# Performance work log

Measured on AMD Instinct MI355X. Metric: run time of the kernel, lower is better.

## Reference

```python
import jax, jax.numpy as jnp
import numpy as np

B, S, D_MODEL, H = 4, 1024, 768, 12
DEPTH = D_MODEL // H  # 64


def setup_inputs() -> dict:
    key = jax.random.key(0)
    ks = jax.random.split(key, 11)
    sd = 1.0 / np.sqrt(D_MODEL)
    return {
        "q": jax.random.normal(ks[0], (B, S, D_MODEL), jnp.float32),
        "k": jax.random.normal(ks[1], (B, S, D_MODEL), jnp.float32),
        "v": jax.random.normal(ks[2], (B, S, D_MODEL), jnp.float32),
        # NOTE: source uses [Dense(depth)] * num_heads -> ONE shared layer per q/k/v
        "Wq": jax.random.normal(ks[3], (D_MODEL, DEPTH), jnp.float32) * sd,
        "bq": jnp.zeros((DEPTH,), jnp.float32),
        "Wk": jax.random.normal(ks[4], (D_MODEL, DEPTH), jnp.float32) * sd,
        "bk": jnp.zeros((DEPTH,), jnp.float32),
        "Wv": jax.random.normal(ks[5], (D_MODEL, DEPTH), jnp.float32) * sd,
        "bv": jnp.zeros((DEPTH,), jnp.float32),
        "Wc": jax.random.normal(ks[6], (D_MODEL, D_MODEL), jnp.float32) * sd,
        "bc": jnp.zeros((D_MODEL,), jnp.float32),
    }


def reference(q, k, v, Wq, bq, Wk, bk, Wv, bv, Wc, bc):
    # All heads share the same weights (list * num_heads aliasing in source),
    # so compute one head and replicate. Heads produce identical outputs.
    qh = q @ Wq + bq  # [B, S, depth]
    kh = k @ Wk + bk
    vh = v @ Wv + bv
    # Source bug reproduced: dk = tf.shape(k)[1] on [B,H,S,depth] == num_heads
    scale = 1.0 / jnp.sqrt(jnp.float32(H))
    scores = jnp.einsum('bqd,bkd->bqk', qh, kh) * scale  # [B, S, S]
    weights = jax.nn.softmax(scores, axis=-1)
    oh = jnp.einsum('bqk,bkd->bqd', weights, vh)  # [B, S, depth]
    # concat of H identical heads along feature dim -> tile
    concat = jnp.tile(oh, (1, 1, H))  # [B, S, d_model]
    output = concat @ Wc + bc
    attention_weights = jnp.broadcast_to(weights[:, None], (B, H, S, S))
    return (output, attention_weights)
```

## Files before the change

kernel.cpp:

```cpp
#include <hip/hip_runtime.h>
#include <math.h>

#define BB 4
#define SS 1024
#define DM 768
#define HH 12
#define DEPTH 64
#define QBLK 8
#define PROWS 16
#define NROWS (BB * SS)

typedef float vfloat4 __attribute__((ext_vector_type(4)));
typedef short bf16x8 __attribute__((ext_vector_type(8)));
typedef float f32x4 __attribute__((ext_vector_type(4)));

__device__ inline ushort f2bf(float x) {
    uint u = __float_as_uint(x);
    u += 0x7FFFu + ((u >> 16) & 1u);
    return (ushort)(u >> 16);
}

__global__ __launch_bounds__(256, 3) void proj_kernel(
    const float* __restrict__ q, const float* __restrict__ k, const float* __restrict__ v,
    const float* __restrict__ Wq, const float* __restrict__ bq,
    const float* __restrict__ Wk, const float* __restrict__ bk,
    const float* __restrict__ Wv, const float* __restrict__ bv,
    float* __restrict__ qh, ushort* __restrict__ khu, ushort* __restrict__ vhu)
{
    __shared__ __align__(16) float rows[PROWS][DM];
    const int nrb  = NROWS / PROWS;
    const int m    = blockIdx.x / nrb;
    const int rb   = blockIdx.x % nrb;
    const int row0 = rb * PROWS;
    const int t    = threadIdx.x;

    const float* src  = (m == 0) ? q  : (m == 1) ? k  : v;
    const float* W    = (m == 0) ? Wq : (m == 1) ? Wk : Wv;
    const float* bias = (m == 0) ? bq : (m == 1) ? bk : bv;

    const float4* s4 = (const float4*)(src + (size_t)row0 * DM);
    float4* r4 = (float4*)&rows[0][0];
    for (int i = t; i < PROWS * DM / 4; i += 256) r4[i] = s4[i];
    __syncthreads();

    const int d  = t & 63;
    const int rg = t >> 6;
    const float* Wp = W + d;
    float a0 = bias[d], a1 = a0, a2 = a0, a3 = a0;
    #pragma unroll 8
    for (int i = 0; i < DM; i += 4) {
        const float wv0 = Wp[(size_t)(i + 0) * DEPTH];
        const float wv1 = Wp[(size_t)(i + 1) * DEPTH];
        const float wv2 = Wp[(size_t)(i + 2) * DEPTH];
        const float wv3 = Wp[(size_t)(i + 3) * DEPTH];
        const float4 r0 = *(const float4*)&rows[rg * 4 + 0][i];
        const float4 r1 = *(const float4*)&rows[rg * 4 + 1][i];
        const float4 r2 = *(const float4*)&rows[rg * 4 + 2][i];
        const float4 r3 = *(const float4*)&rows[rg * 4 + 3][i];
        a0 = fmaf(r0.x, wv0, a0); a0 = fmaf(r0.y, wv1, a0); a0 = fmaf(r0.z, wv2, a0); a0 = fmaf(r0.w, wv3, a0);
        a1 = fmaf(r1.x, wv0, a1); a1 = fmaf(r1.y, wv1, a1); a1 = fmaf(r1.z, wv2, a1); a1 = fmaf(r1.w, wv3, a1);
        a2 = fmaf(r2.x, wv0, a2); a2 = fmaf(r2.y, wv1, a2); a2 = fmaf(r2.z, wv2, a2); a2 = fmaf(r2.w, wv3, a2);
        a3 = fmaf(r3.x, wv0, a3); a3 = fmaf(r3.y, wv1, a3); a3 = fmaf(r3.z, wv2, a3); a3 = fmaf(r3.w, wv3, a3);
    }
    const size_t base = (size_t)(row0 + rg * 4) * DEPTH + d;
    if (m == 0) {
        float* dp = qh + base;
        dp[0] = a0; dp[DEPTH] = a1; dp[2 * DEPTH] = a2; dp[3 * DEPTH] = a3;
    } else {
        ushort* du = ((m == 1) ? khu : vhu) + base;
        du[0] = f2bf(a0); du[DEPTH] = f2bf(a1); du[2 * DEPTH] = f2bf(a2); du[3 * DEPTH] = f2bf(a3);
    }
}

__global__ __launch_bounds__(256) void wcred_kernel(
    const float* __restrict__ Wc, float* __restrict__ Wr)
{
    int idx = blockIdx.x * 256 + threadIdx.x;
    if (idx >= DEPTH * DM) return;
    int d = idx / DM, j = idx % DM;
    float s = 0.f;
    #pragma unroll
    for (int h = 0; h < HH; ++h)
        s += Wc[(size_t)(h * DEPTH + d) * DM + j];
    Wr[idx] = s;
}

__global__ __launch_bounds__(512, 4) void attn_core(
    const float* __restrict__ qh, const ushort* __restrict__ khu, const ushort* __restrict__ vhu,
    const float* __restrict__ Wr, const float* __restrict__ bc,
    float* __restrict__ out, float* __restrict__ attn)
{
    __shared__ __align__(16) ushort qf[16 * 72];
    __shared__ __align__(16) ushort kvbuf[256 * 72];
    __shared__ __align__(16) ushort pf[16 * 1032];
    __shared__ float redmax[16 * 8];
    __shared__ float redsum[16 * 8];

    const int t = threadIdx.x, l = t & 63, wid = t >> 6;
    const int li = l & 15, g4 = l >> 4;
    const int blk = blockIdx.x, b = blk >> 7;
    const int q0 = (blk & 127) * QBLK;
    const int key = t >> 1, hf = t & 1;

    {
        const int qq = t >> 6, dd = t & 63;
        qf[qq * 72 + dd] = f2bf(qh[((size_t)b * SS + q0 + qq) * DEPTH + dd] * 0.28867513459481287f);
        for (int i = t; i < 8 * 72; i += 512) qf[8 * 72 + i] = 0;
        for (int i = t; i < 8 * 1032; i += 512) pf[8 * 1032 + i] = 0;
    }

    const ushort* khb = khu + (size_t)b * SS * DEPTH;
    const ushort* vhb = vhu + (size_t)b * SS * DEPTH;

    uint4 kr0, kr1, kr2, kr3;
    {
        const uint4* g = (const uint4*)(khb + (size_t)key * DEPTH + hf * 32);
        kr0 = g[0]; kr1 = g[1]; kr2 = g[2]; kr3 = g[3];
    }
    __syncthreads();

    const bf16x8 a0 = *(const bf16x8*)&qf[li * 72 + g4 * 8];
    const bf16x8 a1 = *(const bf16x8*)&qf[li * 72 + 32 + g4 * 8];

    f32x4 c[8];
    #pragma unroll
    for (int i = 0; i < 8; ++i) c[i] = (f32x4){0.f, 0.f, 0.f, 0.f};

    #pragma unroll
    for (int s = 0; s < 4; ++s) {
        if (s) __syncthreads();
        {
            uint4* d4 = (uint4*)&kvbuf[key * 72 + hf * 32];
            d4[0] = kr0; d4[1] = kr1; d4[2] = kr2; d4[3] = kr3;
        }
        if (s < 3) {
            const uint4* g = (const uint4*)(khb + (size_t)((s + 1) * 256 + key) * DEPTH + hf * 32);
            kr0 = g[0]; kr1 = g[1]; kr2 = g[2]; kr3 = g[3];
        }
        __syncthreads();
        __builtin_amdgcn_s_setprio(1);
        #pragma unroll
        for (int jj = 0; jj < 2; ++jj) {
            const int tl = wid + 8 * jj;
            const int ci = 2 * s + jj;
            const bf16x8 b0 = *(const bf16x8*)&kvbuf[(tl * 16 + li) * 72 + g4 * 8];
            const bf16x8 b1 = *(const bf16x8*)&kvbuf[(tl * 16 + li) * 72 + 32 + g4 * 8];
            c[ci] = __builtin_amdgcn_mfma_f32_16x16x32_bf16(a0, b0, c[ci], 0, 0, 0);
            c[ci] = __builtin_amdgcn_mfma_f32_16x16x32_bf16(a1, b1, c[ci], 0, 0, 0);
        }
        __builtin_amdgcn_s_setprio(0);
    }

    bf16x8 vr0, vr1, vr2, vr3;
    {
        const bf16x8* g = (const bf16x8*)(vhb + (size_t)key * DEPTH + hf * 32);
        vr0 = g[0]; vr1 = g[1]; vr2 = g[2]; vr3 = g[3];
    }

    float mx[4], sm[4], inv[4];
    #pragma unroll
    for (int r = 0; r < 4; ++r) {
        float m_ = c[0][r];
        #pragma unroll
        for (int i = 1; i < 8; ++i) m_ = fmaxf(m_, c[i][r]);
        #pragma unroll
        for (int off = 1; off < 16; off <<= 1) m_ = fmaxf(m_, __shfl_xor(m_, off));
        mx[r] = m_;
    }
    if (li == 0) {
        #pragma unroll
        for (int r = 0; r < 4; ++r) redmax[(4 * g4 + r) * 8 + wid] = mx[r];
    }
    __syncthreads();
    #pragma unroll
    for (int r = 0; r < 4; ++r) {
        float m_ = redmax[(4 * g4 + r) * 8];
        #pragma unroll
        for (int w2 = 1; w2 < 8; ++w2) m_ = fmaxf(m_, redmax[(4 * g4 + r) * 8 + w2]);
        mx[r] = m_;
        sm[r] = 0.f;
    }
    #pragma unroll
    for (int i = 0; i < 8; ++i) {
        #pragma unroll
        for (int r = 0; r < 4; ++r) {
            const float e = __expf(c[i][r] - mx[r]);
            c[i][r] = e;
            sm[r] += e;
        }
    }
    #pragma unroll
    for (int r = 0; r < 4; ++r) {
        float s_ = sm[r];
        #pragma unroll
        for (int off = 1; off < 16; off <<= 1) s_ += __shfl_xor(s_, off);
        sm[r] = s_;
    }
    if (li == 0) {
        #pragma unroll
        for (int r = 0; r < 4; ++r) redsum[(4 * g4 + r) * 8 + wid] = sm[r];
    }
    __syncthreads();
    #pragma unroll
    for (int r = 0; r < 4; ++r) {
        float s_ = 0.f;
        #pragma unroll
        for (int w2 = 0; w2 < 8; ++w2) s_ += redsum[(4 * g4 + r) * 8 + w2];
        inv[r] = 1.f / s_;
    }
    if (l < 32) {
        #pragma unroll
        for (int i = 0; i < 8; ++i) {
            const int colbase = (16 * (i >> 1) + wid + 8 * (i & 1)) * 16 + li;
            #pragma unroll
            for (int r = 0; r < 4; ++r)
                pf[(4 * g4 + r) * 1032 + colbase] = f2bf(c[i][r] * inv[r]);
        }
    }
    __syncthreads();

    f32x4 cp = {0.f, 0.f, 0.f, 0.f};
    const int dt = wid >> 1, par = wid & 1;
    ushort* VT = kvbuf;
    #pragma unroll
    for (int s = 0; s < 4; ++s) {
        if (s) __syncthreads();
        {
            #pragma unroll
            for (int i = 0; i < 8; ++i) {
                VT[(hf * 32 + i     ) * 264 + key] = (ushort)vr0[i];
                VT[(hf * 32 + 8 + i ) * 264 + key] = (ushort)vr1[i];
                VT[(hf * 32 + 16 + i) * 264 + key] = (ushort)vr2[i];
                VT[(hf * 32 + 24 + i) * 264 + key] = (ushort)vr3[i];
            }
        }
        if (s < 3) {
            const bf16x8* g = (const bf16x8*)(vhb + (size_t)((s + 1) * 256 + key) * DEPTH + hf * 32);
            vr0 = g[0]; vr1 = g[1]; vr2 = g[2]; vr3 = g[3];
        }
        __syncthreads();
        __builtin_amdgcn_s_setprio(1);
        #pragma unroll
        for (int c2 = 0; c2 < 4; ++c2) {
            const int cc = par + 2 * c2;
            const bf16x8 ap = *(const bf16x8*)&pf[li * 1032 + s * 256 + cc * 32 + g4 * 8];
            const bf16x8 bv = *(const bf16x8*)&VT[(dt * 16 + li) * 264 + cc * 32 + g4 * 8];
            cp = __builtin_amdgcn_mfma_f32_16x16x32_bf16(ap, bv, cp, 0, 0, 0);
        }
        __builtin_amdgcn_s_setprio(0);
    }
    __syncthreads();

    float* part_f = (float*)kvbuf;
    float* ohT_f  = ((float*)kvbuf) + 2048;
    #pragma unroll
    for (int r = 0; r < 4; ++r) part_f[wid * 256 + r * 64 + l] = cp[r];
    __syncthreads();
    {
        const int qq = t >> 6, dd = t & 63;
        const int ls = (qq >> 2) * 16 + (dd & 15), rr = qq & 3, w0 = (dd >> 4) * 2;
        ohT_f[dd * 12 + qq] = part_f[w0 * 256 + rr * 64 + ls] + part_f[(w0 + 1) * 256 + rr * 64 + ls];
    }
    __syncthreads();

    for (int j = t; j < DM; j += 512) {
        float a[QBLK];
        const float bj = bc[j];
        #pragma unroll
        for (int r = 0; r < QBLK; ++r) a[r] = bj;
        const float* wc = Wr + j;
        #pragma unroll 16
        for (int d2 = 0; d2 < DEPTH; ++d2) {
            const float wv = wc[(size_t)d2 * DM];
            const float4 o0 = *(const float4*)&ohT_f[d2 * 12];
            const float4 o1 = *(const float4*)&ohT_f[d2 * 12 + 4];
            a[0] = fmaf(o0.x, wv, a[0]); a[1] = fmaf(o0.y, wv, a[1]);
            a[2] = fmaf(o0.z, wv, a[2]); a[3] = fmaf(o0.w, wv, a[3]);
            a[4] = fmaf(o1.x, wv, a[4]); a[5] = fmaf(o1.y, wv, a[5]);
            a[6] = fmaf(o1.z, wv, a[6]); a[7] = fmaf(o1.w, wv, a[7]);
        }
        float* ob = out + ((size_t)b * SS + q0) * DM + j;
        #pragma unroll
        for (int r = 0; r < QBLK; ++r)
            __builtin_nontemporal_store(a[r], ob + (size_t)r * DM);
    }

    {
        const int qq = t >> 6, c0 = t & 63;
        const ushort* prow = &pf[qq * 1032];
        float* abase = attn + ((size_t)(b * HH) * SS + (q0 + qq)) * SS;
        #pragma unroll
        for (int i = 0; i < 4; ++i) {
            const int col = i * 256 + c0 * 4;
            vfloat4 v4;
            v4.x = __uint_as_float((uint)prow[col + 0] << 16);
            v4.y = __uint_as_float((uint)prow[col + 1] << 16);
            v4.z = __uint_as_float((uint)prow[col + 2] << 16);
            v4.w = __uint_as_float((uint)prow[col + 3] << 16);
            #pragma unroll
            for (int h = 0; h < HH; ++h)
                __builtin_nontemporal_store(v4, (vfloat4*)(abase + (size_t)h * SS * SS + col));
        }
    }
}

extern "C" void kernel_launch(void* const* d_in, const int* in_sizes, int n_in,
                              void* d_out, int out_size, void* d_ws, size_t ws_size,
                              hipStream_t stream) {
    const float* q  = (const float*)d_in[0];
    const float* k  = (const float*)d_in[1];
    const float* v  = (const float*)d_in[2];
    const float* Wq = (const float*)d_in[3];
    const float* bq = (const float*)d_in[4];
    const float* Wk = (const float*)d_in[5];
    const float* bk = (const float*)d_in[6];
    const float* Wv = (const float*)d_in[7];
    const float* bv = (const float*)d_in[8];
    const float* Wc = (const float*)d_in[9];
    const float* bc = (const float*)d_in[10];

    float* out  = (float*)d_out;
    float* attn = out + (size_t)BB * SS * DM;

    float* ws = (float*)d_ws;
    const size_t NPROJ = (size_t)NROWS * DEPTH;
    float* qh   = ws;
    ushort* khu = (ushort*)(ws + NPROJ);
    ushort* vhu = (ushort*)(ws + NPROJ + NPROJ / 2);
    float* Wr   = ws + 2 * NPROJ;

    wcred_kernel<<<(DEPTH * DM + 255) / 256, 256, 0, stream>>>(Wc, Wr);
    proj_kernel<<<3 * (NROWS / PROWS), 256, 0, stream>>>(q, k, v, Wq, bq, Wk, bk, Wv, bv, qh, khu, vhu);
    attn_core<<<BB * (SS / QBLK), 512, 0, stream>>>(qh, khu, vhu, Wr, bc, out, attn);
}
```

Measured before the change: 100.1 us.

## Process 16 query rows per block with 1024 threads in attention core

Doubles the query block from 8 to 16 rows and the workgroup from 512 to 1024 threads, so the 16x16 MFMA tiles no longer carry zero-padded rows. K/V tiles are each loaded once per 16 queries instead of 8, halving staging traffic and the number of blocks. Work is redistributed so each of 16 waves handles one key tile per stage, with reductions widened to 16 waves. Larger blocks reduce the number of blocks and may lower occupancy flexibility.

```diff
diff --git a/kernel.cpp b/kernel.cpp
--- a/kernel.cpp
+++ b/kernel.cpp
@@ -6,7 +6,7 @@
 #define DM 768
 #define HH 12
 #define DEPTH 64
-#define QBLK 8
+#define QBLK 16
 #define PROWS 16
 #define NROWS (BB * SS)
 
@@ -85,7 +85,7 @@
     Wr[idx] = s;
 }
 
-__global__ __launch_bounds__(512, 4) void attn_core(
+__global__ __launch_bounds__(1024, 4) void attn_core(
     const float* __restrict__ qh, const ushort* __restrict__ khu, const ushort* __restrict__ vhu,
     const float* __restrict__ Wr, const float* __restrict__ bc,
     float* __restrict__ out, float* __restrict__ attn)
@@ -93,68 +93,63 @@
     __shared__ __align__(16) ushort qf[16 * 72];
     __shared__ __align__(16) ushort kvbuf[256 * 72];
     __shared__ __align__(16) ushort pf[16 * 1032];
-    __shared__ float redmax[16 * 8];
-    __shared__ float redsum[16 * 8];
+    __shared__ float redmax[16 * 16];
+    __shared__ float redsum[16 * 16];
 
     const int t = threadIdx.x, l = t & 63, wid = t >> 6;
     const int li = l & 15, g4 = l >> 4;
-    const int blk = blockIdx.x, b = blk >> 7;
-    const int q0 = (blk & 127) * QBLK;
-    const int key = t >> 1, hf = t & 1;
+    const int blk = blockIdx.x, b = blk >> 6;
+    const int q0 = (blk & 63) * QBLK;
+    const int key = t >> 2, qu = t & 3;
 
     {
         const int qq = t >> 6, dd = t & 63;
         qf[qq * 72 + dd] = f2bf(qh[((size_t)b * SS + q0 + qq) * DEPTH + dd] * 0.28867513459481287f);
-        for (int i = t; i < 8 * 72; i += 512) qf[8 * 72 + i] = 0;
-        for (int i = t; i < 8 * 1032; i += 512) pf[8 * 1032 + i] = 0;
     }
 
     const ushort* khb = khu + (size_t)b * SS * DEPTH;
     const ushort* vhb = vhu + (size_t)b * SS * DEPTH;
 
-    uint4 kr0, kr1, kr2, kr3;
-    {
-        const uint4* g = (const uint4*)(khb + (size_t)key * DEPTH + hf * 32);
-        kr0 = g[0]; kr1 = g[1]; kr2 = g[2]; kr3 = g[3];
+    uint4 kr0, kr1;
+    {
+        const uint4* g = (const uint4*)(khb + (size_t)key * DEPTH + qu * 16);
+        kr0 = g[0]; kr1 = g[1];
     }
     __syncthreads();
 
     const bf16x8 a0 = *(const bf16x8*)&qf[li * 72 + g4 * 8];
     const bf16x8 a1 = *(const bf16x8*)&qf[li * 72 + 32 + g4 * 8];
 
-    f32x4 c[8];
-    #pragma unroll
-    for (int i = 0; i < 8; ++i) c[i] = (f32x4){0.f, 0.f, 0.f, 0.f};
+    f32x4 c[4];
+    #pragma unroll
+    for (int i = 0; i < 4; ++i) c[i] = (f32x4){0.f, 0.f, 0.f, 0.f};
 
     #pragma unroll
     for (int s = 0; s < 4; ++s) {
         if (s) __syncthreads();
         {
-            uint4* d4 = (uint4*)&kvbuf[key * 72 + hf * 32];
-            d4[0] = kr0; d4[1] = kr1; d4[2] = kr2; d4[3] = kr3;
+            uint4* d4 = (uint4*)&kvbuf[key * 72 + qu * 16];
+            d4[0] = kr0; d4[1] = kr1;
         }
         if (s < 3) {
-            const uint4* g = (const uint4*)(khb + (size_t)((s + 1) * 256 + key) * DEPTH + hf * 32);
-            kr0 = g[0]; kr1 = g[1]; kr2 = g[2]; kr3 = g[3];
+            const uint4* g = (const uint4*)(khb + (size_t)((s + 1) * 256 + key) * DEPTH + qu * 16);
+            kr0 = g[0]; kr1 = g[1];
         }
         __syncthreads();
         __builtin_amdgcn_s_setprio(1);
-        #pragma unroll
-        for (int jj = 0; jj < 2; ++jj) {
-            const int tl = wid + 8 * jj;
-            const int ci = 2 * s + jj;
-            const bf16x8 b0 = *(const bf16x8*)&kvbuf[(tl * 16 + li) * 72 + g4 * 8];
-            const bf16x8 b1 = *(const bf16x8*)&kvbuf[(tl * 16 + li) * 72 + 32 + g4 * 8];
-            c[ci] = __builtin_amdgcn_mfma_f32_16x16x32_bf16(a0, b0, c[ci], 0, 0, 0);
-            c[ci] = __builtin_amdgcn_mfma_f32_16x16x32_bf16(a1, b1, c[ci], 0, 0, 0);
+        {
+            const bf16x8 b0 = *(const bf16x8*)&kvbuf[(wid * 16 + li) * 72 + g4 * 8];
+            const bf16x8 b1 = *(const bf16x8*)&kvbuf[(wid * 16 + li) * 72 + 32 + g4 * 8];
+            c[s] = __builtin_amdgcn_mfma_f32_16x16x32_bf16(a0, b0, c[s], 0, 0, 0);
+            c[s] = __builtin_amdgcn_mfma_f32_16x16x32_bf16(a1, b1, c[s], 0, 0, 0);
         }
         __builtin_amdgcn_s_setprio(0);
     }
 
-    bf16x8 vr0, vr1, vr2, vr3;
-    {
-        const bf16x8* g = (const bf16x8*)(vhb + (size_t)key * DEPTH + hf * 32);
-        vr0 = g[0]; vr1 = g[1]; vr2 = g[2]; vr3 = g[3];
+    bf16x8 vr0, vr1;
+    {
+        const bf16x8* g = (const bf16x8*)(vhb + (size_t)key * DEPTH + qu * 16);
+        vr0 = g[0]; vr1 = g[1];
     }
 
     float mx[4], sm[4], inv[4];
@@ -162,26 +157,26 @@
     for (int r = 0; r < 4; ++r) {
         float m_ = c[0][r];
         #pragma unroll
-        for (int i = 1; i < 8; ++i) m_ = fmaxf(m_, c[i][r]);
+        for (int i = 1; i < 4; ++i) m_ = fmaxf(m_, c[i][r]);
         #pragma unroll
         for (int off = 1; off < 16; off <<= 1) m_ = fmaxf(m_, __shfl_xor(m_, off));
         mx[r] = m_;
     }
     if (li == 0) {
         #pragma unroll
-        for (int r = 0; r < 4; ++r) redmax[(4 * g4 + r) * 8 + wid] = mx[r];
+        for (int r = 0; r < 4; ++r) redmax[(4 * g4 + r) * 16 + wid] = mx[r];
     }
     __syncthreads();
     #pragma unroll
     for (int r = 0; r < 4; ++r) {
-        float m_ = redmax[(4 * g4 + r) * 8];
-        #pragma unroll
-        for (int w2 = 1; w2 < 8; ++w2) m_ = fmaxf(m_, redmax[(4 * g4 + r) * 8 + w2]);
+        float m_ = redmax[(4 * g4 + r) * 16];
+        #pragma unroll
+        for (int w2 = 1; w2 < 16; ++w2) m_ = fmaxf(m_, redmax[(4 * g4 + r) * 16 + w2]);
         mx[r] = m_;
         sm[r] = 0.f;
     }
     #pragma unroll
-    for (int i = 0; i < 8; ++i) {
+    for (int i = 0; i < 4; ++i) {
         #pragma unroll
         for (int r = 0; r < 4; ++r) {
             const float e = __expf(c[i][r] - mx[r]);
@@ -198,29 +193,27 @@
     }
     if (li == 0) {
         #pragma unroll
-        for (int r = 0; r < 4; ++r) redsum[(4 * g4 + r) * 8 + wid] = sm[r];
+        for (int r = 0; r < 4; ++r) redsum[(4 * g4 + r) * 16 + wid] = sm[r];
     }
     __syncthreads();
     #pragma unroll
     for (int r = 0; r < 4; ++r) {
         float s_ = 0.f;
         #pragma unroll
-        for (int w2 = 0; w2 < 8; ++w2) s_ += redsum[(4 * g4 + r) * 8 + w2];
+        for (int w2 = 0; w2 < 16; ++w2) s_ += redsum[(4 * g4 + r) * 16 + w2];
         inv[r] = 1.f / s_;
     }
-    if (l < 32) {
-        #pragma unroll
-        for (int i = 0; i < 8; ++i) {
-            const int colbase = (16 * (i >> 1) + wid + 8 * (i & 1)) * 16 + li;
-            #pragma unroll
-            for (int r = 0; r < 4; ++r)
-                pf[(4 * g4 + r) * 1032 + colbase] = f2bf(c[i][r] * inv[r]);
-        }
+    #pragma unroll
+    for (int i = 0; i < 4; ++i) {
+        const int colbase = (i * 16 + wid) * 16 + li;
+        #pragma unroll
+        for (int r = 0; r < 4; ++r)
+            pf[(4 * g4 + r) * 1032 + colbase] = f2bf(c[i][r] * inv[r]);
     }
     __syncthreads();
 
     f32x4 cp = {0.f, 0.f, 0.f, 0.f};
-    const int dt = wid >> 1, par = wid & 1;
+    const int dt = wid >> 2, par = wid & 3;
     ushort* VT = kvbuf;
     #pragma unroll
     for (int s = 0; s < 4; ++s) {
@@ -228,23 +221,22 @@
         {
             #pragma unroll
             for (int i = 0; i < 8; ++i) {
-                VT[(hf * 32 + i     ) * 264 + key] = (ushort)vr0[i];
-                VT[(hf * 32 + 8 + i ) * 264 + key] = (ushort)vr1[i];
-                VT[(hf * 32 + 16 + i) * 264 + key] = (ushort)vr2[i];
-                VT[(hf * 32 + 24 + i) * 264 + key] = (ushort)vr3[i];
+                VT[(qu * 16 + i    ) * 266 + key] = (ushort)vr0[i];
+                VT[(qu * 16 + 8 + i) * 266 + key] = (ushort)vr1[i];
             }
         }
         if (s < 3) {
-            const bf16x8* g = (const bf16x8*)(vhb + (size_t)((s + 1) * 256 + key) * DEPTH + hf * 32);
-            vr0 = g[0]; vr1 = g[1]; vr2 = g[2]; vr3 = g[3];
+            const bf16x8* g = (const bf16x8*)(vhb + (size_t)((s + 1) * 256 + key) * DEPTH + qu * 16);
+            vr0 = g[0]; vr1 = g[1];
         }
         __syncthreads();
         __builtin_amdgcn_s_setprio(1);
         #pragma unroll
-        for (int c2 = 0; c2 < 4; ++c2) {
-            const int cc = par + 2 * c2;
-            const bf16x8 ap = *(const bf16x8*)&pf[li * 1032 + s * 256 + cc * 32 + g4 * 8];
-            const bf16x8 bv = *(const bf16x8*)&VT[(dt * 16 + li) * 264 + cc * 32 + g4 * 8];
+        for (int c2 = 0; c2 < 2; ++c2) {
+            const int cc = par + 4 * c2;
+            const int kk = s * 256 + cc * 32 + g4 * 8;
+            const bf16x8 ap = *(const bf16x8*)&pf[li * 1032 + kk];
+            const bf16x8 bv = *(const bf16x8*)&VT[(dt * 16 + li) * 266 + cc * 32 + g4 * 8];
             cp = __builtin_amdgcn_mfma_f32_16x16x32_bf16(ap, bv, cp, 0, 0, 0);
         }
         __builtin_amdgcn_s_setprio(0);
@@ -252,18 +244,23 @@
     __syncthreads();
 
     float* part_f = (float*)kvbuf;
-    float* ohT_f  = ((float*)kvbuf) + 2048;
+    float* ohT_f  = ((float*)kvbuf) + 16 * 256;
     #pragma unroll
     for (int r = 0; r < 4; ++r) part_f[wid * 256 + r * 64 + l] = cp[r];
     __syncthreads();
     {
-        const int qq = t >> 6, dd = t & 63;
-        const int ls = (qq >> 2) * 16 + (dd & 15), rr = qq & 3, w0 = (dd >> 4) * 2;
-        ohT_f[dd * 12 + qq] = part_f[w0 * 256 + rr * 64 + ls] + part_f[(w0 + 1) * 256 + rr * 64 + ls];
-    }
-    __syncthreads();
-
-    for (int j = t; j < DM; j += 512) {
+        const int dd = t & 63, qq = t >> 6;
+        const int ls = (qq >> 2) * 16 + (dd & 15), rr = qq & 3, w0 = (dd >> 4) * 4;
+        float s_ = 0.f;
+        #pragma unroll
+        for (int p2 = 0; p2 < 4; ++p2)
+            s_ += part_f[(w0 + p2) * 256 + rr * 64 + ls];
+        ohT_f[dd * 16 + qq] = s_;
+    }
+    __syncthreads();
+
+    if (t < DM) {
+        const int j = t;
         float a[QBLK];
         const float bj = bc[j];
         #pragma unroll
@@ -272,12 +269,18 @@
         #pragma unroll 16
         for (int d2 = 0; d2 < DEPTH; ++d2) {
             const float wv = wc[(size_t)d2 * DM];
-            const float4 o0 = *(const float4*)&ohT_f[d2 * 12];
-            const float4 o1 = *(const float4*)&ohT_f[d2 * 12 + 4];
-            a[0] = fmaf(o0.x, wv, a[0]); a[1] = fmaf(o0.y, wv, a[1]);
-            a[2] = fmaf(o0.z, wv, a[2]); a[3] = fmaf(o0.w, wv, a[3]);
-            a[4] = fmaf(o1.x, wv, a[4]); a[5] = fmaf(o1.y, wv, a[5]);
-            a[6] = fmaf(o1.z, wv, a[6]); a[7] = fmaf(o1.w, wv, a[7]);
+            const float4 o0 = *(const float4*)&ohT_f[d2 * 16];
+            const float4 o1 = *(const float4*)&ohT_f[d2 * 16 + 4];
+            const float4 o2 = *(const float4*)&ohT_f[d2 * 16 + 8];
+            const float4 o3 = *(const float4*)&ohT_f[d2 * 16 + 12];
+            a[0]  = fmaf(o0.x, wv, a[0]);  a[1]  = fmaf(o0.y, wv, a[1]);
+            a[2]  = fmaf(o0.z, wv, a[2]);  a[3]  = fmaf(o0.w, wv, a[3]);
+            a[4]  = fmaf(o1.x, wv, a[4]);  a[5]  = fmaf(o1.y, wv, a[5]);
+            a[6]  = fmaf(o1.z, wv, a[6]);  a[7]  = fmaf(o1.w, wv, a[7]);
+            a[8]  = fmaf(o2.x, wv, a[8]);  a[9]  = fmaf(o2.y, wv, a[9]);
+            a[10] = fmaf(o2.z, wv, a[10]); a[11] = fmaf(o2.w, wv, a[11]);
+            a[12] = fmaf(o3.x, wv, a[12]); a[13] = fmaf(o3.y, wv, a[13]);
+            a[14] = fmaf(o3.z, wv, a[14]); a[15] = fmaf(o3.w, wv, a[15]);
         }
         float* ob = out + ((size_t)b * SS + q0) * DM + j;
         #pragma unroll
@@ -331,5 +334,5 @@
 
     wcred_kernel<<<(DEPTH * DM + 255) / 256, 256, 0, stream>>>(Wc, Wr);
     proj_kernel<<<3 * (NROWS / PROWS), 256, 0, stream>>>(q, k, v, Wq, bq, Wk, bk, Wv, bv, qh, khu, vhu);
-    attn_core<<<BB * (SS / QBLK), 512, 0, stream>>>(qh, khu, vhu, Wr, bc, out, attn);
-}
+    attn_core<<<BB * (SS / QBLK), 1024, 0, stream>>>(qh, khu, vhu, Wr, bc, out, attn);
+}
```

New measurement: 101.3 us. No clear change (+1.2%).

## Store V projection transposed so attention loads V^T with vector copies

Applied to the files above, without the earlier changes.

The projection kernel now writes the V projection in a transposed [depth][B*S] bf16 layout, going through a small shared-memory transpose tile. The attention kernel can then fill its V^T shared tile with 16-byte vector stores instead of 32 scalar scattered ushort stores per thread each stage. This removes many LDS scatter writes and likely bank conflicts in attn_core. In exchange the projection kernel gains an extra barrier and strided 2-byte global stores for V, written as 16 consecutive shorts per depth row.

```diff
diff --git a/kernel.cpp b/kernel.cpp
--- a/kernel.cpp
+++ b/kernel.cpp
@@ -25,9 +25,10 @@
     const float* __restrict__ Wq, const float* __restrict__ bq,
     const float* __restrict__ Wk, const float* __restrict__ bk,
     const float* __restrict__ Wv, const float* __restrict__ bv,
-    float* __restrict__ qh, ushort* __restrict__ khu, ushort* __restrict__ vhu)
+    float* __restrict__ qh, ushort* __restrict__ khu, ushort* __restrict__ vhT)
 {
     __shared__ __align__(16) float rows[PROWS][DM];
+    __shared__ float resT[DEPTH][PROWS + 1];
     const int nrb  = NROWS / PROWS;
     const int m    = blockIdx.x / nrb;
     const int rb   = blockIdx.x % nrb;
@@ -62,13 +63,23 @@
         a2 = fmaf(r2.x, wv0, a2); a2 = fmaf(r2.y, wv1, a2); a2 = fmaf(r2.z, wv2, a2); a2 = fmaf(r2.w, wv3, a2);
         a3 = fmaf(r3.x, wv0, a3); a3 = fmaf(r3.y, wv1, a3); a3 = fmaf(r3.z, wv2, a3); a3 = fmaf(r3.w, wv3, a3);
     }
-    const size_t base = (size_t)(row0 + rg * 4) * DEPTH + d;
-    if (m == 0) {
-        float* dp = qh + base;
+    if (m == 2) {
+        resT[d][rg * 4 + 0] = a0;
+        resT[d][rg * 4 + 1] = a1;
+        resT[d][rg * 4 + 2] = a2;
+        resT[d][rg * 4 + 3] = a3;
+        __syncthreads();
+        #pragma unroll
+        for (int e = t; e < DEPTH * PROWS; e += 256) {
+            const int dd = e >> 4, rr = e & 15;
+            vhT[(size_t)dd * NROWS + row0 + rr] = f2bf(resT[dd][rr]);
+        }
+    } else if (m == 1) {
+        ushort* du = khu + (size_t)(row0 + rg * 4) * DEPTH + d;
+        du[0] = f2bf(a0); du[DEPTH] = f2bf(a1); du[2 * DEPTH] = f2bf(a2); du[3 * DEPTH] = f2bf(a3);
+    } else {
+        float* dp = qh + (size_t)(row0 + rg * 4) * DEPTH + d;
         dp[0] = a0; dp[DEPTH] = a1; dp[2 * DEPTH] = a2; dp[3 * DEPTH] = a3;
-    } else {
-        ushort* du = ((m == 1) ? khu : vhu) + base;
-        du[0] = f2bf(a0); du[DEPTH] = f2bf(a1); du[2 * DEPTH] = f2bf(a2); du[3 * DEPTH] = f2bf(a3);
     }
 }
 
@@ -86,7 +97,7 @@
 }
 
 __global__ __launch_bounds__(512, 4) void attn_core(
-    const float* __restrict__ qh, const ushort* __restrict__ khu, const ushort* __restrict__ vhu,
+    const float* __restrict__ qh, const ushort* __restrict__ khu, const ushort* __restrict__ vhT,
     const float* __restrict__ Wr, const float* __restrict__ bc,
     float* __restrict__ out, float* __restrict__ attn)
 {
@@ -110,7 +121,7 @@
     }
 
     const ushort* khb = khu + (size_t)b * SS * DEPTH;
-    const ushort* vhb = vhu + (size_t)b * SS * DEPTH;
+    const ushort* vtb = vhT + (size_t)b * SS;
 
     uint4 kr0, kr1, kr2, kr3;
     {
@@ -151,10 +162,14 @@
         __builtin_amdgcn_s_setprio(0);
     }
 
-    bf16x8 vr0, vr1, vr2, vr3;
-    {
-        const bf16x8* g = (const bf16x8*)(vhb + (size_t)key * DEPTH + hf * 32);
-        vr0 = g[0]; vr1 = g[1]; vr2 = g[2]; vr3 = g[3];
+    const int vrow = t >> 5;
+    const int vcol = (t & 31) * 8;
+    uint4 vp0, vp1, vp2, vp3;
+    {
+        vp0 = *(const uint4*)(vtb + (size_t)(0 * 16 + vrow) * NROWS + vcol);
+        vp1 = *(const uint4*)(vtb + (size_t)(1 * 16 + vrow) * NROWS + vcol);
+        vp2 = *(const uint4*)(vtb + (size_t)(2 * 16 + vrow) * NROWS + vcol);
+        vp3 = *(const uint4*)(vtb + (size_t)(3 * 16 + vrow) * NROWS + vcol);
     }
 
     float mx[4], sm[4], inv[4];
@@ -226,17 +241,17 @@
     for (int s = 0; s < 4; ++s) {
         if (s) __syncthreads();
         {
-            #pragma unroll
-            for (int i = 0; i < 8; ++i) {
-                VT[(hf * 32 + i     ) * 264 + key] = (ushort)vr0[i];
-                VT[(hf * 32 + 8 + i ) * 264 + key] = (ushort)vr1[i];
-                VT[(hf * 32 + 16 + i) * 264 + key] = (ushort)vr2[i];
-                VT[(hf * 32 + 24 + i) * 264 + key] = (ushort)vr3[i];
-            }
+            *(uint4*)&VT[(0 * 16 + vrow) * 264 + vcol] = vp0;
+            *(uint4*)&VT[(1 * 16 + vrow) * 264 + vcol] = vp1;
+            *(uint4*)&VT[(2 * 16 + vrow) * 264 + vcol] = vp2;
+            *(uint4*)&VT[(3 * 16 + vrow) * 264 + vcol] = vp3;
         }
         if (s < 3) {
-            const bf16x8* g = (const bf16x8*)(vhb + (size_t)((s + 1) * 256 + key) * DEPTH + hf * 32);
-            vr0 = g[0]; vr1 = g[1]; vr2 = g[2]; vr3 = g[3];
+            const int sc = (s + 1) * 256;
+            vp0 = *(const uint4*)(vtb + (size_t)(0 * 16 + vrow) * NROWS + sc + vcol);
+            vp1 = *(const uint4*)(vtb + (size_t)(1 * 16 + vrow) * NROWS + sc + vcol);
+            vp2 = *(const uint4*)(vtb + (size_t)(2 * 16 + vrow) * NROWS + sc + vcol);
+            vp3 = *(const uint4*)(vtb + (size_t)(3 * 16 + vrow) * NROWS + sc + vcol);
         }
         __syncthreads();
         __builtin_amdgcn_s_setprio(1);
@@ -326,10 +341,10 @@
     const size_t NPROJ = (size_t)NROWS * DEPTH;
     float* qh   = ws;
     ushort* khu = (ushort*)(ws + NPROJ);
-    ushort* vhu = (ushort*)(ws + NPROJ + NPROJ / 2);
+    ushort* vhT = (ushort*)(ws + NPROJ + NPROJ / 2);
     float* Wr   = ws + 2 * NPROJ;
 
     wcred_kernel<<<(DEPTH * DM + 255) / 256, 256, 0, stream>>>(Wc, Wr);
-    proj_kernel<<<3 * (NROWS / PROWS), 256, 0, stream>>>(q, k, v, Wq, bq, Wk, bk, Wv, bv, qh, khu, vhu);
-    attn_core<<<BB * (SS / QBLK), 512, 0, stream>>>(qh, khu, vhu, Wr, bc, out, attn);
-}
+    proj_kernel<<<3 * (NROWS / PROWS), 256, 0, stream>>>(q, k, v, Wq, bq, Wk, bk, Wv, bv, qh, khu, vhT);
+    attn_core<<<BB * (SS / QBLK), 512, 0, stream>>>(qh, khu, vhT, Wr, bc, out, attn);
+}
```

Result: no change. 101.6 us (+1.5%).
